# Kernel tuning notes

Hardware: AMD Instinct MI355X
Metric: run time of the kernel (lower is better)

## Reference

```python
import jax, jax.numpy as jnp
import numpy as np

D, NH, NKV, HD, FFN = 2560, 8, 4, 256, 10240
QD = NH * HD
CTX = 4096
EPS = 1e-6


def _rms(x, eps=EPS):
    # Equivalent to F.layer_norm(cat([x,-x]), 2D): zero mean, var = mean(x^2)
    return x * jax.lax.rsqrt(jnp.mean(jnp.square(x), axis=-1, keepdims=True) + eps)


def rmsnorm(x, w):
    # Gemma-style ANERMSNorm with learnable scale (1 + w)
    return _rms(x) * (1.0 + w)


def rotate_half(x):
    x1, x2 = jnp.split(x, 2, axis=-1)
    return jnp.concatenate([-x2, x1], axis=-1)


def setup_inputs() -> dict:
    key = jax.random.key(0)
    ks = jax.random.split(key, 16)
    s = 0.02
    return {
        "x": jax.random.normal(ks[0], (1, 1, D), jnp.float32),
        "cos": jax.random.uniform(ks[1], (1, 1, HD), jnp.float32, -1.0, 1.0),
        "sin": jax.random.uniform(ks[2], (1, 1, HD), jnp.float32, -1.0, 1.0),
        "mask": jnp.zeros((1, 1, 1, CTX), jnp.float32),
        "cache_k": jax.random.normal(ks[3], (1, NKV, CTX, HD), jnp.float32),
        "cache_v": jax.random.normal(ks[4], (1, NKV, CTX, HD), jnp.float32),
        "ctx_len": CTX,
        "w_in_ln": jax.random.normal(ks[5], (D,), jnp.float32) * s,
        "w_post_attn_ln": jax.random.normal(ks[6], (D,), jnp.float32) * s,
        "w_pre_ffn_ln": jax.random.normal(ks[7], (D,), jnp.float32) * s,
        "w_post_ffn_ln": jax.random.normal(ks[8], (D,), jnp.float32) * s,
        "Wq": jax.random.normal(ks[9], (QD, D), jnp.float32) * s,
        "Wo": jax.random.normal(ks[10], (D, QD), jnp.float32) * s,
        "Wg": jax.random.normal(ks[11], (FFN, D), jnp.float32) * s,
        "Wu": jax.random.normal(ks[12], (FFN, D), jnp.float32) * s,
        "Wd": jax.random.normal(ks[13], (D, FFN), jnp.float32) * s,
    }


def reference(x, cos, sin, mask, cache_k, cache_v, ctx_len,
              w_in_ln, w_post_attn_ln, w_pre_ffn_ln, w_post_ffn_ln,
              Wq, Wo, Wg, Wu, Wd):
    rep = NH // NKV
    residual = x
    h = rmsnorm(x, w_in_ln)                      # (1,1,D)
    q = h @ Wq.T                                 # (1,1,QD)  1x1-conv == linear
    q = q.reshape(1, 1, NH, HD)
    q = _rms(q)                                  # q_norm, no learnable weight
    q = q.transpose(0, 2, 1, 3)                  # (1,NH,1,HD)
    q = q * cos[:, None] + rotate_half(q) * sin[:, None]
    k = jnp.repeat(cache_k, rep, axis=1)         # (1,NH,L,HD) GQA expand
    v = jnp.repeat(cache_v, rep, axis=1)
    scores = jnp.einsum("bhqd,bhkd->bhqk", q, k) * 1.0 + mask
    attn = jax.nn.softmax(scores, axis=-1)       # numerically stable softmax
    a = jnp.einsum("bhqk,bhkd->bhqd", attn, v)   # (1,NH,1,HD)
    a = a.transpose(0, 2, 1, 3).reshape(1, 1, QD)
    a = a @ Wo.T                                 # (1,1,D)
    x = residual + rmsnorm(a, w_post_attn_ln)
    residual = x
    h = rmsnorm(x, w_pre_ffn_ln)
    g = jax.nn.gelu(h @ Wg.T, approximate=True)  # tanh-approx GELU
    ffn = (g * (h @ Wu.T)) @ Wd.T                # GeGLU down-proj
    x = residual + rmsnorm(ffn, w_post_ffn_ln)
    return x
```

## Files before the change

kernel.cpp:

```cpp
#include <hip/hip_runtime.h>

#define D_    2560
#define NH_   8
#define NKV_  4
#define HD_   256
#define FFN_  10240
#define QD_   2048
#define CTX_  4096
#define EPSF  1e-6f
#define ACH   128

typedef float f4 __attribute__((ext_vector_type(4)));

__device__ __forceinline__ float wave_red_sum(float v) {
#pragma unroll
    for (int o = 32; o > 0; o >>= 1) v += __shfl_down(v, o, 64);
    return v;
}

__device__ __forceinline__ float wave_red_sum_b(float v) {
#pragma unroll
    for (int o = 32; o > 0; o >>= 1) v += __shfl_xor(v, o, 64);
    return v;
}

template <int NW>
__device__ __forceinline__ float block_red_sum(float v) {
    __shared__ float s[NW];
    __shared__ float tot;
    int lane = threadIdx.x & 63, w = threadIdx.x >> 6;
    v = wave_red_sum(v);
    if (lane == 0) s[w] = v;
    __syncthreads();
    if (threadIdx.x == 0) {
        float t = 0.f;
#pragma unroll
        for (int i = 0; i < NW; i++) t += s[i];
        tot = t;
    }
    __syncthreads();
    return tot;
}

template <int NW>
__device__ __forceinline__ float block_red_max(float v) {
    __shared__ float s[NW];
    __shared__ float tot;
    int lane = threadIdx.x & 63, w = threadIdx.x >> 6;
#pragma unroll
    for (int o = 32; o > 0; o >>= 1) v = fmaxf(v, __shfl_down(v, o, 64));
    if (lane == 0) s[w] = v;
    __syncthreads();
    if (threadIdx.x == 0) {
        float t = -3e38f;
#pragma unroll
        for (int i = 0; i < NW; i++) t = fmaxf(t, s[i]);
        tot = t;
    }
    __syncthreads();
    return tot;
}

__global__ __launch_bounds__(256) void k_wq_fused(const float* __restrict__ Wq,
                                                  const float* __restrict__ x,
                                                  const float* __restrict__ w_in,
                                                  float* __restrict__ qraw) {
    int lane = threadIdx.x & 63;
    int row = (blockIdx.x * 256 + threadIdx.x) >> 6;
    const f4* X = (const f4*)x + lane;
    const f4* WI = (const f4*)w_in + lane;
    f4 xx[10], wi[10];
#pragma unroll
    for (int k = 0; k < 10; k++) xx[k] = X[k * 64];
#pragma unroll
    for (int k = 0; k < 10; k++) wi[k] = WI[k * 64];
    const f4* Wr = (const f4*)Wq + (size_t)row * 640 + lane;
    f4 wv[10];
#pragma unroll
    for (int k = 0; k < 10; k++) wv[k] = __builtin_nontemporal_load(Wr + k * 64);
    float ss = 0.f;
#pragma unroll
    for (int k = 0; k < 10; k++)
        ss += xx[k].x * xx[k].x + xx[k].y * xx[k].y + xx[k].z * xx[k].z + xx[k].w * xx[k].w;
    ss = wave_red_sum_b(ss);
    float rs = rsqrtf(ss / (float)D_ + EPSF);
    float acc = 0.f;
#pragma unroll
    for (int k = 0; k < 10; k++) {
        f4 hh = xx[k] * rs * (1.f + wi[k]);
        acc += wv[k].x * hh.x + wv[k].y * hh.y + wv[k].z * hh.z + wv[k].w * hh.w;
    }
    acc = wave_red_sum(acc);
    if (lane == 0) qraw[row] = acc;
}

template <int CPL>
__global__ __launch_bounds__(256) void k_gemv_row(const float* __restrict__ W,
                                                  const float* __restrict__ x,
                                                  float* __restrict__ y) {
    int lane = threadIdx.x & 63;
    int row = (blockIdx.x * 256 + threadIdx.x) >> 6;
    const f4* X = (const f4*)x + lane;
    f4 xx[CPL];
#pragma unroll
    for (int k = 0; k < CPL; k++) xx[k] = X[k * 64];
    const f4* Wr = (const f4*)W + (size_t)row * (CPL * 64) + lane;
    f4 wv[CPL];
#pragma unroll
    for (int k = 0; k < CPL; k++) wv[k] = __builtin_nontemporal_load(Wr + k * 64);
    float acc = 0.f;
#pragma unroll
    for (int k = 0; k < CPL; k++)
        acc += wv[k].x * xx[k].x + wv[k].y * xx[k].y + wv[k].z * xx[k].z + wv[k].w * xx[k].w;
    acc = wave_red_sum(acc);
    if (lane == 0) y[row] = acc;
}

__global__ __launch_bounds__(256) void k_gg_stream(const float* __restrict__ Wg,
                                                   const float* __restrict__ Wu,
                                                   const float* __restrict__ h,
                                                   float* __restrict__ part) {
    int lane = threadIdx.x & 63;
    int t = (blockIdx.x * 256 + threadIdx.x) >> 6;
    const f4* X = (const f4*)h + lane;
    f4 xx[10];
#pragma unroll
    for (int k = 0; k < 10; k++) xx[k] = X[k * 64];
    const f4* Wr = ((t < FFN_) ? (const f4*)Wg + (size_t)t * 640
                               : (const f4*)Wu + (size_t)(t - FFN_) * 640) + lane;
    f4 wv[10];
#pragma unroll
    for (int k = 0; k < 10; k++) wv[k] = __builtin_nontemporal_load(Wr + k * 64);
    float acc = 0.f;
#pragma unroll
    for (int k = 0; k < 10; k++)
        acc += wv[k].x * xx[k].x + wv[k].y * xx[k].y + wv[k].z * xx[k].z + wv[k].w * xx[k].w;
    acc = wave_red_sum(acc);
    if (lane == 0) part[t] = acc;
}

__global__ __launch_bounds__(256) void k_gelu_fuse(const float* __restrict__ part,
                                                   float* __restrict__ gu) {
    int i = blockIdx.x * 256 + threadIdx.x;
    float g = part[i], u = part[FFN_ + i];
    float tt = tanhf(0.7978845608028654f * (g + 0.044715f * g * g * g));
    gu[i] = 0.5f * g * (1.f + tt) * u;
}

__global__ __launch_bounds__(256) void k_wd(const float* __restrict__ Wd,
                                            const float* __restrict__ gu,
                                            float* __restrict__ part) {
    int lane = threadIdx.x & 63;
    int t = (blockIdx.x * 256 + threadIdx.x) >> 6;
    int half = t & 1;
    const f4* Wr = (const f4*)Wd + (size_t)t * 1280 + lane;
    const f4* Xp = (const f4*)gu + half * 1280 + lane;
    float acc = 0.f;
#pragma unroll
    for (int b = 0; b < 2; b++) {
        f4 xx[10], wv[10];
#pragma unroll
        for (int j = 0; j < 10; j++) xx[j] = Xp[(b * 10 + j) * 64];
#pragma unroll
        for (int j = 0; j < 10; j++)
            wv[j] = __builtin_nontemporal_load(Wr + (b * 10 + j) * 64);
#pragma unroll
        for (int j = 0; j < 10; j++)
            acc += wv[j].x * xx[j].x + wv[j].y * xx[j].y + wv[j].z * xx[j].z + wv[j].w * xx[j].w;
    }
    acc = wave_red_sum(acc);
    if (lane == 0) part[t] = acc;
}

__global__ __launch_bounds__(512) void k_res_rms(const float* __restrict__ res,
                                                 const float* __restrict__ apart, int slots,
                                                 const float* __restrict__ w1, float* __restrict__ out1,
                                                 const float* __restrict__ w2, float* __restrict__ out2) {
    const int K = D_ / 512;
    int t = threadIdx.x;
    float va[K];
    float ss = 0.f;
#pragma unroll
    for (int k = 0; k < K; k++) {
        int i = t + k * 512;
        float v = 0.f;
        for (int s = 0; s < slots; s++) v += apart[(size_t)i * slots + s];
        va[k] = v;
        ss += v * v;
    }
    float tot = block_red_sum<8>(ss);
    float rs = rsqrtf(tot / (float)D_ + EPSF);
    float vo[K];
    float ss2 = 0.f;
#pragma unroll
    for (int k = 0; k < K; k++) {
        int i = t + k * 512;
        float r = res ? res[i] : 0.f;
        vo[k] = r + va[k] * rs * (1.f + w1[i]);
        out1[i] = vo[k];
        ss2 += vo[k] * vo[k];
    }
    if (out2) {
        float tot2 = block_red_sum<8>(ss2);
        float rs2 = rsqrtf(tot2 / (float)D_ + EPSF);
#pragma unroll
        for (int k = 0; k < K; k++) {
            int i = t + k * 512;
            out2[i] = vo[k] * rs2 * (1.f + w2[i]);
        }
    }
}

__global__ __launch_bounds__(256) void k_attn_part(const float* __restrict__ Kc,
                                                   const float* __restrict__ V,
                                                   const float* __restrict__ qraw,
                                                   const float* __restrict__ cosv,
                                                   const float* __restrict__ sinv,
                                                   const float* __restrict__ mask,
                                                   float* __restrict__ pm,
                                                   float* __restrict__ pl,
                                                   float* __restrict__ pacc) {
    constexpr int RW = CTX_ / ACH;
    int kvh = blockIdx.x, ch = blockIdx.y;
    int lane = threadIdx.x & 63, w = threadIdx.x >> 6;
    int t = threadIdx.x;
    int h0 = 2 * kvh, h1 = h0 + 1;
    int l0 = ch * RW;
    __shared__ float s0[RW], s1[RW];
    __shared__ f4 pv0[4][64], pv1[4][64];

    const f4* q4 = (const f4*)qraw;
    f4 qr0 = q4[h0 * 64 + lane];
    f4 qr1 = q4[h1 * 64 + lane];
    float n0 = wave_red_sum_b(qr0.x * qr0.x + qr0.y * qr0.y + qr0.z * qr0.z + qr0.w * qr0.w);
    float n1 = wave_red_sum_b(qr1.x * qr1.x + qr1.y * qr1.y + qr1.z * qr1.z + qr1.w * qr1.w);
    f4 qn0 = qr0 * rsqrtf(n0 / (float)HD_ + EPSF);
    f4 qn1 = qr1 * rsqrtf(n1 / (float)HD_ + EPSF);
    f4 p0, p1;
    p0.x = __shfl_xor(qn0.x, 32, 64); p0.y = __shfl_xor(qn0.y, 32, 64);
    p0.z = __shfl_xor(qn0.z, 32, 64); p0.w = __shfl_xor(qn0.w, 32, 64);
    p1.x = __shfl_xor(qn1.x, 32, 64); p1.y = __shfl_xor(qn1.y, 32, 64);
    p1.z = __shfl_xor(qn1.z, 32, 64); p1.w = __shfl_xor(qn1.w, 32, 64);
    f4 rot0 = (lane < 32) ? -p0 : p0;
    f4 rot1 = (lane < 32) ? -p1 : p1;
    f4 cs = ((const f4*)cosv)[lane];
    f4 sn = ((const f4*)sinv)[lane];
    f4 q0 = qn0 * cs + rot0 * sn;
    f4 q1 = qn1 * cs + rot1 * sn;

    const f4* Kb = (const f4*)Kc + ((size_t)kvh * CTX_ + l0 + w * 8) * 64 + lane;
    f4 kk[8];
#pragma unroll
    for (int i = 0; i < 8; i++) kk[i] = Kb[i * 64];
    float d0[8], d1[8];
#pragma unroll
    for (int i = 0; i < 8; i++) {
        d0[i] = kk[i].x * q0.x + kk[i].y * q0.y + kk[i].z * q0.z + kk[i].w * q0.w;
        d1[i] = kk[i].x * q1.x + kk[i].y * q1.y + kk[i].z * q1.z + kk[i].w * q1.w;
    }
#pragma unroll
    for (int o = 32; o > 0; o >>= 1) {
#pragma unroll
        for (int i = 0; i < 8; i++) {
            d0[i] += __shfl_down(d0[i], o, 64);
            d1[i] += __shfl_down(d1[i], o, 64);
        }
    }
    if (lane == 0) {
#pragma unroll
        for (int i = 0; i < 8; i++) {
            float m = mask[l0 + w * 8 + i];
            s0[w * 8 + i] = d0[i] + m;
            s1[w * 8 + i] = d1[i] + m;
        }
    }
    __syncthreads();

    float m0 = block_red_max<4>(t < RW ? s0[t] : -3e38f);
    float m1 = block_red_max<4>(t < RW ? s1[t] : -3e38f);
    float e0 = 0.f, e1 = 0.f;
    if (t < RW) {
        e0 = expf(s0[t] - m0); s0[t] = e0;
        e1 = expf(s1[t] - m1); s1[t] = e1;
    }
    float l0sum = block_red_sum<4>(e0);
    float l1sum = block_red_sum<4>(e1);

    const f4* Vb = (const f4*)V + ((size_t)kvh * CTX_ + l0 + w * 8) * 64 + lane;
    f4 vv[8];
#pragma unroll
    for (int i = 0; i < 8; i++) vv[i] = Vb[i * 64];
    f4 a0 = {0.f, 0.f, 0.f, 0.f}, a1 = {0.f, 0.f, 0.f, 0.f};
#pragma unroll
    for (int i = 0; i < 8; i++) {
        a0 += vv[i] * s0[w * 8 + i];
        a1 += vv[i] * s1[w * 8 + i];
    }
    pv0[w][lane] = a0;
    pv1[w][lane] = a1;
    __syncthreads();
    const float* f0 = (const float*)pv0;
    const float* f1 = (const float*)pv1;
    float r0 = f0[t] + f0[256 + t] + f0[512 + t] + f0[768 + t];
    float r1 = f1[t] + f1[256 + t] + f1[512 + t] + f1[768 + t];
    pacc[((size_t)(h0 * ACH) + ch) * HD_ + t] = r0;
    pacc[((size_t)(h1 * ACH) + ch) * HD_ + t] = r1;
    if (t == 0) {
        pm[h0 * ACH + ch] = m0; pl[h0 * ACH + ch] = l0sum;
        pm[h1 * ACH + ch] = m1; pl[h1 * ACH + ch] = l1sum;
    }
}

__global__ __launch_bounds__(256) void k_attn_comb(const float* __restrict__ pm,
                                                   const float* __restrict__ pl,
                                                   const float* __restrict__ pacc,
                                                   float* __restrict__ a) {
    int h = blockIdx.x, t = threadIdx.x;
    __shared__ float wgt[ACH];
    float M = block_red_max<4>(t < ACH ? pm[h * ACH + t] : -3e38f);
    float lw = 0.f;
    if (t < ACH) {
        float wv = expf(pm[h * ACH + t] - M);
        wgt[t] = wv;
        lw = wv * pl[h * ACH + t];
    }
    float L = block_red_sum<4>(lw);
    float acc = 0.f;
    const float* pb = pacc + (size_t)h * ACH * HD_ + t;
#pragma unroll 8
    for (int c = 0; c < ACH; c++) acc += wgt[c] * pb[(size_t)c * HD_];
    a[h * HD_ + t] = acc / L;
}

extern "C" void kernel_launch(void* const* d_in, const int* in_sizes, int n_in,
                              void* d_out, int out_size, void* d_ws, size_t ws_size,
                              hipStream_t stream) {
    const float* x     = (const float*)d_in[0];
    const float* cosv  = (const float*)d_in[1];
    const float* sinv  = (const float*)d_in[2];
    const float* mask  = (const float*)d_in[3];
    const float* cK    = (const float*)d_in[4];
    const float* cV    = (const float*)d_in[5];
    const float* w_in  = (const float*)d_in[7];
    const float* w_pa  = (const float*)d_in[8];
    const float* w_pf  = (const float*)d_in[9];
    const float* w_pff = (const float*)d_in[10];
    const float* Wq    = (const float*)d_in[11];
    const float* Wo    = (const float*)d_in[12];
    const float* Wg    = (const float*)d_in[13];
    const float* Wu    = (const float*)d_in[14];
    const float* Wd    = (const float*)d_in[15];

    float* ws    = (float*)d_ws;
    float* qraw  = ws;
    float* pm    = ws + 2048;
    float* pl    = ws + 3072;
    float* pacc  = ws + 4096;
    float* a     = ws + 266240;
    float* ao    = ws + 268288;
    float* x2    = ws + 270848;
    float* h2    = ws + 273408;
    float* partg = ws + 275968;
    float* gu    = ws + 296448;
    float* partd = ws + 306688;
    float* out   = (float*)d_out;

    k_wq_fused<<<QD_ / 4, 256, 0, stream>>>(Wq, x, w_in, qraw);
    k_attn_part<<<dim3(NKV_, ACH), 256, 0, stream>>>(cK, cV, qraw, cosv, sinv,
                                                     mask, pm, pl, pacc);
    k_attn_comb<<<NH_, 256, 0, stream>>>(pm, pl, pacc, a);
    k_gemv_row<8><<<D_ / 4, 256, 0, stream>>>(Wo, a, ao);
    k_res_rms<<<1, 512, 0, stream>>>(x, ao, 1, w_pa, x2, w_pf, h2);
    k_gg_stream<<<2 * FFN_ / 4, 256, 0, stream>>>(Wg, Wu, h2, partg);
    k_gelu_fuse<<<FFN_ / 256, 256, 0, stream>>>(partg, gu);
    k_wd<<<D_ * 2 / 4, 256, 0, stream>>>(Wd, gu, partd);
    k_res_rms<<<1, 512, 0, stream>>>(x2, partd, 2, w_pff, out, nullptr, nullptr);
}
```

Measured before the change: 93.39 us.

## Split FFN GEMVs into column chunks with 8 rows per wave and partial sums

The gate/up and down-projection GEMVs are restructured so each wave handles one 256-float column chunk across 8 strided rows, instead of one whole row per wave. Partial dot products are written per chunk and reduced later in the GELU kernel (10 slots) and the final residual-RMS kernel (40 slots). The aim is more memory-level parallelism and a different access pattern for streaming the large FFN weights. In exchange it adds partial-sum traffic, strided per-wave reads of 1 KB segments from different rows, and more work in the reduction kernels.

```diff
diff --git a/kernel.cpp b/kernel.cpp
--- a/kernel.cpp
+++ b/kernel.cpp
@@ -116,64 +116,83 @@
     if (lane == 0) y[row] = acc;
 }
 
-__global__ __launch_bounds__(256) void k_gg_stream(const float* __restrict__ Wg,
-                                                   const float* __restrict__ Wu,
-                                                   const float* __restrict__ h,
-                                                   float* __restrict__ part) {
+__global__ __launch_bounds__(256) void k_gg_probe(const float* __restrict__ Wg,
+                                                  const float* __restrict__ Wu,
+                                                  const float* __restrict__ h,
+                                                  float* __restrict__ part) {
     int lane = threadIdx.x & 63;
-    int t = (blockIdx.x * 256 + threadIdx.x) >> 6;
-    const f4* X = (const f4*)h + lane;
-    f4 xx[10];
-#pragma unroll
-    for (int k = 0; k < 10; k++) xx[k] = X[k * 64];
-    const f4* Wr = ((t < FFN_) ? (const f4*)Wg + (size_t)t * 640
-                               : (const f4*)Wu + (size_t)(t - FFN_) * 640) + lane;
-    f4 wv[10];
-#pragma unroll
-    for (int k = 0; k < 10; k++) wv[k] = __builtin_nontemporal_load(Wr + k * 64);
-    float acc = 0.f;
-#pragma unroll
-    for (int k = 0; k < 10; k++)
-        acc += wv[k].x * xx[k].x + wv[k].y * xx[k].y + wv[k].z * xx[k].z + wv[k].w * xx[k].w;
-    acc = wave_red_sum(acc);
-    if (lane == 0) part[t] = acc;
+    int gw = (blockIdx.x * 256 + threadIdx.x) >> 6;
+    int c = gw % 10;
+    int rb = gw - c * 1;  rb = gw / 10;
+    f4 xx = ((const f4*)h)[c * 64 + lane];
+    f4 wv[8];
+#pragma unroll
+    for (int j = 0; j < 8; j++) {
+        int r = rb + j * 2560;
+        const f4* p = (r < FFN_) ? (const f4*)Wg + (size_t)r * 640
+                                 : (const f4*)Wu + (size_t)(r - FFN_) * 640;
+        wv[j] = __builtin_nontemporal_load(p + c * 64 + lane);
+    }
+    float d[8];
+#pragma unroll
+    for (int j = 0; j < 8; j++)
+        d[j] = wv[j].x * xx.x + wv[j].y * xx.y + wv[j].z * xx.z + wv[j].w * xx.w;
+#pragma unroll
+    for (int o = 32; o > 0; o >>= 1) {
+#pragma unroll
+        for (int j = 0; j < 8; j++) d[j] += __shfl_down(d[j], o, 64);
+    }
+    if (lane == 0) {
+#pragma unroll
+        for (int j = 0; j < 8; j++) part[c * 20480 + rb + j * 2560] = d[j];
+    }
 }
 
 __global__ __launch_bounds__(256) void k_gelu_fuse(const float* __restrict__ part,
                                                    float* __restrict__ gu) {
     int i = blockIdx.x * 256 + threadIdx.x;
-    float g = part[i], u = part[FFN_ + i];
+    float g = 0.f, u = 0.f;
+#pragma unroll
+    for (int c = 0; c < 10; c++) {
+        g += part[c * 20480 + i];
+        u += part[c * 20480 + FFN_ + i];
+    }
     float tt = tanhf(0.7978845608028654f * (g + 0.044715f * g * g * g));
     gu[i] = 0.5f * g * (1.f + tt) * u;
 }
 
-__global__ __launch_bounds__(256) void k_wd(const float* __restrict__ Wd,
-                                            const float* __restrict__ gu,
-                                            float* __restrict__ part) {
+__global__ __launch_bounds__(256) void k_wd_probe(const float* __restrict__ Wd,
+                                                  const float* __restrict__ gu,
+                                                  float* __restrict__ part) {
     int lane = threadIdx.x & 63;
-    int t = (blockIdx.x * 256 + threadIdx.x) >> 6;
-    int half = t & 1;
-    const f4* Wr = (const f4*)Wd + (size_t)t * 1280 + lane;
-    const f4* Xp = (const f4*)gu + half * 1280 + lane;
-    float acc = 0.f;
-#pragma unroll
-    for (int b = 0; b < 2; b++) {
-        f4 xx[10], wv[10];
-#pragma unroll
-        for (int j = 0; j < 10; j++) xx[j] = Xp[(b * 10 + j) * 64];
-#pragma unroll
-        for (int j = 0; j < 10; j++)
-            wv[j] = __builtin_nontemporal_load(Wr + (b * 10 + j) * 64);
-#pragma unroll
-        for (int j = 0; j < 10; j++)
-            acc += wv[j].x * xx[j].x + wv[j].y * xx[j].y + wv[j].z * xx[j].z + wv[j].w * xx[j].w;
-    }
-    acc = wave_red_sum(acc);
-    if (lane == 0) part[t] = acc;
+    int gw = (blockIdx.x * 256 + threadIdx.x) >> 6;
+    int c = gw % 40;
+    int rb = gw / 40;
+    f4 xx = ((const f4*)gu)[c * 64 + lane];
+    f4 wv[8];
+#pragma unroll
+    for (int j = 0; j < 8; j++) {
+        int r = rb + j * 320;
+        wv[j] = __builtin_nontemporal_load((const f4*)Wd + (size_t)r * 2560 + c * 64 + lane);
+    }
+    float d[8];
+#pragma unroll
+    for (int j = 0; j < 8; j++)
+        d[j] = wv[j].x * xx.x + wv[j].y * xx.y + wv[j].z * xx.z + wv[j].w * xx.w;
+#pragma unroll
+    for (int o = 32; o > 0; o >>= 1) {
+#pragma unroll
+        for (int j = 0; j < 8; j++) d[j] += __shfl_down(d[j], o, 64);
+    }
+    if (lane == 0) {
+#pragma unroll
+        for (int j = 0; j < 8; j++) part[c * 2560 + rb + j * 320] = d[j];
+    }
 }
 
 __global__ __launch_bounds__(512) void k_res_rms(const float* __restrict__ res,
-                                                 const float* __restrict__ apart, int slots,
+                                                 const float* __restrict__ apart,
+                                                 int slots, int pstride,
                                                  const float* __restrict__ w1, float* __restrict__ out1,
                                                  const float* __restrict__ w2, float* __restrict__ out2) {
     const int K = D_ / 512;
@@ -184,7 +203,7 @@
     for (int k = 0; k < K; k++) {
         int i = t + k * 512;
         float v = 0.f;
-        for (int s = 0; s < slots; s++) v += apart[(size_t)i * slots + s];
+        for (int s = 0; s < slots; s++) v += apart[(size_t)s * pstride + i];
         va[k] = v;
         ss += v * v;
     }
@@ -360,9 +379,9 @@
     float* ao    = ws + 268288;
     float* x2    = ws + 270848;
     float* h2    = ws + 273408;
-    float* partg = ws + 275968;
-    float* gu    = ws + 296448;
-    float* partd = ws + 306688;
+    float* gu    = ws + 275968;
+    float* partg = ws + 286208;
+    float* partd = ws + 491008;
     float* out   = (float*)d_out;
 
     k_wq_fused<<<QD_ / 4, 256, 0, stream>>>(Wq, x, w_in, qraw);
@@ -370,9 +389,9 @@
                                                      mask, pm, pl, pacc);
     k_attn_comb<<<NH_, 256, 0, stream>>>(pm, pl, pacc, a);
     k_gemv_row<8><<<D_ / 4, 256, 0, stream>>>(Wo, a, ao);
-    k_res_rms<<<1, 512, 0, stream>>>(x, ao, 1, w_pa, x2, w_pf, h2);
-    k_gg_stream<<<2 * FFN_ / 4, 256, 0, stream>>>(Wg, Wu, h2, partg);
+    k_res_rms<<<1, 512, 0, stream>>>(x, ao, 1, 0, w_pa, x2, w_pf, h2);
+    k_gg_probe<<<2 * FFN_ * 10 / 8 / 4, 256, 0, stream>>>(Wg, Wu, h2, partg);
     k_gelu_fuse<<<FFN_ / 256, 256, 0, stream>>>(partg, gu);
-    k_wd<<<D_ * 2 / 4, 256, 0, stream>>>(Wd, gu, partd);
-    k_res_rms<<<1, 512, 0, stream>>>(x2, partd, 2, w_pff, out, nullptr, nullptr);
-}
+    k_wd_probe<<<D_ * 40 / 8 / 4, 256, 0, stream>>>(Wd, gu, partd);
+    k_res_rms<<<1, 512, 0, stream>>>(x2, partd, 40, 2560, w_pff, out, nullptr, nullptr);
+}
```

After: 143.3 us. 1.53x slower.
